# Kernel tuning notes

Measured on AMD Instinct MI355X. Metric: run time of the kernel, lower is better.

The kernel has to match this reference:

```python
import jax, jax.numpy as jnp
import numpy as np

HOP = 256
SEG = 1024


def setup_inputs() -> dict:
    key = jax.random.key(0)
    k1, k2, k3 = jax.random.split(key, 3)
    B, N = 16, 2 ** 21
    x = jax.random.normal(k1, (B, N), dtype=jnp.float32)
    analysis_window = jax.random.uniform(k2, (SEG,), dtype=jnp.float32)
    synthesis_window = jax.random.uniform(k3, (SEG,), dtype=jnp.float32)
    return {"x": x, "analysis_window": analysis_window, "synthesis_window": synthesis_window}


def reference(x, analysis_window, synthesis_window):
    """Round trip: segment (windowed framing) then unsegment (overlap-add).

    Faithful to SegmenterTensorFlow.segment + .unsegment, but vectorized:
    a single strided gather-multiply and a single batched scatter-add
    instead of per-frame Python loops.
    """
    B, N = x.shape
    num_segments = (N - SEG) // HOP + 1  # compute_num_segments
    # frame index matrix [num_segments, SEG]
    idx = jnp.arange(num_segments)[:, None] * HOP + jnp.arange(SEG)[None, :]
    # --- segment: X[b,k,j] = x[b, k*hop + j] * analysis_window[j] ---
    X = x[:, idx] * analysis_window  # [B, num_segments, SEG]
    # --- unsegment: overlap-add with synthesis window ---
    num_samples = (num_segments - 1) * HOP + SEG  # compute_num_samples
    y = jnp.zeros((B, num_samples), dtype=X.dtype)
    y = y.at[:, idx].add(X * synthesis_window)  # parallel scatter-add
    return y
```

## Files before the change

### kernel.cpp

```cpp
#include <hip/hip_runtime.h>

#define HOP 256
#define SEG 1024

__global__ __launch_bounds__(256) void SegmenterTensorFlow_28698971472345_kernel(
    const float* __restrict__ x,
    const float* __restrict__ aw,
    const float* __restrict__ sw,
    float* __restrict__ y,
    int n_mask,
    int total4,
    int kmax)
{
    int tid = blockIdx.x * blockDim.x + threadIdx.x;
    int stride = gridDim.x * blockDim.x;

    int r = (tid * 4) & (HOP - 1);

    float4 s[4];
#pragma unroll
    for (int m = 0; m < 4; ++m) {
        const float* pa = aw + r + m * HOP;
        const float* ps = sw + r + m * HOP;
        s[m] = make_float4(pa[0] * ps[0], pa[1] * ps[1], pa[2] * ps[2], pa[3] * ps[3]);
    }

    const float4* __restrict__ x4 = reinterpret_cast<const float4*>(x);
    float4* __restrict__ y4 = reinterpret_cast<float4*>(y);

    for (int t = tid; t < total4; t += stride) {
        int pos = (t * 4) & n_mask;
        int blk = pos >> 8;

        float4 xv = x4[t];

        float wx = 0.f, wy = 0.f, wz = 0.f, ww = 0.f;
#pragma unroll
        for (int m = 0; m < 4; ++m) {
            if (blk >= m && (blk - m) <= kmax) {
                wx += s[m].x; wy += s[m].y; wz += s[m].z; ww += s[m].w;
            }
        }

        float4 o;
        o.x = xv.x * wx;
        o.y = xv.y * wy;
        o.z = xv.z * wz;
        o.w = xv.w * ww;
        y4[t] = o;
    }
}

extern "C" void kernel_launch(void* const* d_in, const int* in_sizes, int n_in,
                              void* d_out, int out_size, void* d_ws, size_t ws_size,
                              hipStream_t stream) {
    const float* x  = (const float*)d_in[0];
    const float* aw = (const float*)d_in[1];
    const float* sw = (const float*)d_in[2];
    float* y = (float*)d_out;

    const int N = 1 << 21;
    const int total4 = out_size / 4;
    const int kmax = (N - SEG) / HOP;

    dim3 block(256);
    dim3 grid(4096);

    SegmenterTensorFlow_28698971472345_kernel<<<grid, block, 0, stream>>>(
        x, aw, sw, y, N - 1, total4, kmax);
}
```

Before: 236.1 us.

## Precompute per-thread window once, unroll loads eight-deep, use nontemporal stores

Removes the grid-stride loop: each thread now handles eight float4 elements spaced by the grid stride, so every element keeps the same in-row position and the overlap-add window weight is computed once per thread. All eight loads are issued before any store to raise memory-level parallelism, and results go out as nontemporal stores to limit cache pollution. Grid size is now derived from total4, which assumes it divides exactly by BLOCK*UNROLL and that N is a multiple of the stride so the weight stays constant across the unrolled elements.

```diff
diff --git a/kernel.cpp b/kernel.cpp
--- a/kernel.cpp
+++ b/kernel.cpp
@@ -2,53 +2,48 @@
 
 #define HOP 256
 #define SEG 1024
+#define BLOCK 256
+#define UNROLL 8
 
-__global__ __launch_bounds__(256) void SegmenterTensorFlow_28698971472345_kernel(
-    const float* __restrict__ x,
+typedef float f32x4 __attribute__((ext_vector_type(4)));
+
+__global__ __launch_bounds__(BLOCK) void SegmenterTensorFlow_28698971472345_kernel(
+    const f32x4* __restrict__ x4,
     const float* __restrict__ aw,
     const float* __restrict__ sw,
-    float* __restrict__ y,
+    f32x4* __restrict__ y4,
     int n_mask,
-    int total4,
     int kmax)
 {
-    int tid = blockIdx.x * blockDim.x + threadIdx.x;
-    int stride = gridDim.x * blockDim.x;
+    const int tid    = blockIdx.x * BLOCK + threadIdx.x;
+    const int stride = gridDim.x * BLOCK;
 
-    int r = (tid * 4) & (HOP - 1);
+    const int pos = (tid * 4) & n_mask;
+    const int r   = pos & (HOP - 1);
+    const int blk = pos >> 8;
 
-    float4 s[4];
+    float wx = 0.f, wy = 0.f, wz = 0.f, ww = 0.f;
 #pragma unroll
     for (int m = 0; m < 4; ++m) {
-        const float* pa = aw + r + m * HOP;
-        const float* ps = sw + r + m * HOP;
-        s[m] = make_float4(pa[0] * ps[0], pa[1] * ps[1], pa[2] * ps[2], pa[3] * ps[3]);
+        if (blk >= m && (blk - m) <= kmax) {
+            const float* pa = aw + r + m * HOP;
+            const float* ps = sw + r + m * HOP;
+            wx += pa[0] * ps[0];
+            wy += pa[1] * ps[1];
+            wz += pa[2] * ps[2];
+            ww += pa[3] * ps[3];
+        }
     }
+    const f32x4 w = {wx, wy, wz, ww};
 
-    const float4* __restrict__ x4 = reinterpret_cast<const float4*>(x);
-    float4* __restrict__ y4 = reinterpret_cast<float4*>(y);
+    f32x4 xv[UNROLL];
+#pragma unroll
+    for (int u = 0; u < UNROLL; ++u)
+        xv[u] = x4[tid + u * stride];
 
-    for (int t = tid; t < total4; t += stride) {
-        int pos = (t * 4) & n_mask;
-        int blk = pos >> 8;
-
-        float4 xv = x4[t];
-
-        float wx = 0.f, wy = 0.f, wz = 0.f, ww = 0.f;
 #pragma unroll
-        for (int m = 0; m < 4; ++m) {
-            if (blk >= m && (blk - m) <= kmax) {
-                wx += s[m].x; wy += s[m].y; wz += s[m].z; ww += s[m].w;
-            }
-        }
-
-        float4 o;
-        o.x = xv.x * wx;
-        o.y = xv.y * wy;
-        o.z = xv.z * wz;
-        o.w = xv.w * ww;
-        y4[t] = o;
-    }
+    for (int u = 0; u < UNROLL; ++u)
+        __builtin_nontemporal_store(xv[u] * w, &y4[tid + u * stride]);
 }
 
 extern "C" void kernel_launch(void* const* d_in, const int* in_sizes, int n_in,
@@ -57,15 +52,14 @@
     const float* x  = (const float*)d_in[0];
     const float* aw = (const float*)d_in[1];
     const float* sw = (const float*)d_in[2];
-    float* y = (float*)d_out;
 
     const int N = 1 << 21;
     const int total4 = out_size / 4;
     const int kmax = (N - SEG) / HOP;
 
-    dim3 block(256);
-    dim3 grid(4096);
+    dim3 block(BLOCK);
+    dim3 grid(total4 / (BLOCK * UNROLL));
 
     SegmenterTensorFlow_28698971472345_kernel<<<grid, block, 0, stream>>>(
-        x, aw, sw, y, N - 1, total4, kmax);
+        (const f32x4*)x, aw, sw, (f32x4*)d_out, N - 1, kmax);
 }
```

Result: no change. 235.6 us (-0.2%).
